# Performance work log

Hardware: AMD Instinct MI355X
Metric: run time of the kernel (lower is better)

The kernel has to match this reference:

```python
import jax, jax.numpy as jnp
import numpy as np

N, K, D, DOUT = 100000, 16, 128, 128

def setup_inputs() -> dict:
    key = jax.random.key(0)
    k1, k2, k3 = jax.random.split(key, 3)
    self_vecs = jax.random.normal(k1, (N, D), dtype=jnp.float32)
    neigh_vecs = jax.random.normal(k2, (N, K, D), dtype=jnp.float32)
    # glorot([input_dim, output_dim])
    limit = np.sqrt(6.0 / (D + DOUT)).astype(np.float32)
    weights = jax.random.uniform(k3, (D, DOUT), dtype=jnp.float32, minval=-limit, maxval=limit)
    return {"self_vecs": self_vecs, "neigh_vecs": neigh_vecs, "weights": weights}

def reference(self_vecs, neigh_vecs, weights):
    # concat self node as an extra "neighbor": [N, K+1, D]
    neigh_self = jnp.concatenate([neigh_vecs, self_vecs[:, None, :]], axis=1)
    # attention scores: query is the self vector, keys are neighbors+self -> [N, K+1]
    score = jnp.einsum('nd,nkd->nk', self_vecs, neigh_self)
    attn = jax.nn.softmax(score, axis=-1)
    # weighted sum of values -> [N, D]
    context = jnp.einsum('nk,nkd->nd', attn, neigh_self)
    out = context @ weights  # [N, DOUT]
    return jax.nn.relu(out)
```

## Files before the change

kernel.cpp:

```cpp
#include <hip/hip_runtime.h>


constexpr int K    = 16;
constexpr int D    = 128;
constexpr int DOUT = 128;
constexpr int WT_PITCH = 136;

typedef short bfrag  __attribute__((ext_vector_type(8)));
typedef float afrag  __attribute__((ext_vector_type(4)));

__device__ __forceinline__ unsigned short f2bf(float f) {
    union { float f; unsigned u; } v; v.f = f;
    const unsigned r = v.u + 0x7FFF + ((v.u >> 16) & 1);
    return (unsigned short)(r >> 16);
}
__device__ __forceinline__ float bf2f(unsigned short b) {
    union { unsigned u; float f; } v; v.u = ((unsigned)b) << 16;
    return v.f;
}

__device__ __forceinline__ float half_allsum(float x) {
    #pragma unroll
    for (int off = 1; off <= 16; off <<= 1)
        x += __shfl_xor(x, off);
    return x;
}

__launch_bounds__(512, 2)
__global__ void gat_fused(const float* __restrict__ self_vecs,
                          const float* __restrict__ neigh_vecs,
                          const float* __restrict__ W,
                          float* __restrict__ out,
                          int n_tiles) {
    __shared__ __align__(16) unsigned short Wt[DOUT][WT_PITCH];
    __shared__ __align__(16) unsigned short Chl[2][2][16][WT_PITCH];

    const int tid = threadIdx.x;

    for (int e = tid; e < D * DOUT; e += blockDim.x) {
        const int k = e >> 7, m = e & 127;
        Wt[m][k] = f2bf(W[e]);
    }
    __syncthreads();

    const int lane = tid & 63;
    const int wid  = tid >> 6;
    const int half = lane >> 5;
    const int q    = lane & 31;
    const int nl   = lane & 15;
    const int kb   = lane >> 4;
    const int r0   = wid * 2;

    float4 v[K], sv;

    int buf = 0;
    int t = blockIdx.x;

    if (t < n_tiles) {
        const int n0 = t * 16 + r0 + half;
        const float4* nb = (const float4*)(neigh_vecs + (size_t)n0 * (K * D)) + q;
        #pragma unroll
        for (int k = 0; k < K; ++k) v[k] = nb[k * 32];
        sv = ((const float4*)(self_vecs + (size_t)n0 * D))[q];
    }

    for (; t < n_tiles; t += gridDim.x, buf ^= 1) {
        const int node0 = t * 16;

        float ss = sv.x * sv.x + sv.y * sv.y + sv.z * sv.z + sv.w * sv.w;
        float sc[K];
        #pragma unroll
        for (int k = 0; k < K; ++k)
            sc[k] = sv.x * v[k].x + sv.y * v[k].y + sv.z * v[k].z + sv.w * v[k].w;
        ss = half_allsum(ss);
        #pragma unroll
        for (int k = 0; k < K; ++k) sc[k] = half_allsum(sc[k]);

        float m = ss;
        #pragma unroll
        for (int k = 0; k < K; ++k) m = fmaxf(m, sc[k]);
        float e   = __expf(ss - m);
        float sum = e;
        float4 cx = make_float4(e * sv.x, e * sv.y, e * sv.z, e * sv.w);
        #pragma unroll
        for (int k = 0; k < K; ++k) {
            const float ek = __expf(sc[k] - m);
            sum += ek;
            cx.x += ek * v[k].x; cx.y += ek * v[k].y;
            cx.z += ek * v[k].z; cx.w += ek * v[k].w;
        }
        const float inv = 1.f / sum;
        const float cf[4] = {cx.x * inv, cx.y * inv, cx.z * inv, cx.w * inv};

        unsigned short hi4[4], lo4[4];
        #pragma unroll
        for (int i = 0; i < 4; ++i) {
            hi4[i] = f2bf(cf[i]);
            lo4[i] = f2bf(cf[i] - bf2f(hi4[i]));
        }
        *(uint2*)&Chl[buf][0][r0 + half][4 * q] = *(const uint2*)hi4;
        *(uint2*)&Chl[buf][1][r0 + half][4 * q] = *(const uint2*)lo4;

        const int tn = t + gridDim.x;
        if (tn < n_tiles) {
            const int n0 = tn * 16 + r0 + half;
            const float4* nb = (const float4*)(neigh_vecs + (size_t)n0 * (K * D)) + q;
            #pragma unroll
            for (int k = 0; k < K; ++k) v[k] = nb[k * 32];
            sv = ((const float4*)(self_vecs + (size_t)n0 * D))[q];
        }

        __syncthreads();

        afrag acc;
        #pragma unroll
        for (int r4 = 0; r4 < 4; ++r4) acc[r4] = 0.f;

        #pragma unroll
        for (int kc = 0; kc < 4; ++kc) {
            const bfrag ch = *(const bfrag*)&Chl[buf][0][nl][kc * 32 + kb * 8];
            const bfrag cl = *(const bfrag*)&Chl[buf][1][nl][kc * 32 + kb * 8];
            const bfrag a  = *(const bfrag*)&Wt[wid * 16 + nl][kc * 32 + kb * 8];
            acc = __builtin_amdgcn_mfma_f32_16x16x32_bf16(a, ch, acc, 0, 0, 0);
            acc = __builtin_amdgcn_mfma_f32_16x16x32_bf16(a, cl, acc, 0, 0, 0);
        }
        float* orow = out + (size_t)(node0 + nl) * DOUT + kb * 4;
        *(float4*)(orow + wid * 16) =
            make_float4(fmaxf(acc[0], 0.f), fmaxf(acc[1], 0.f),
                        fmaxf(acc[2], 0.f), fmaxf(acc[3], 0.f));
    }
}

extern "C" void kernel_launch(void* const* d_in, const int* in_sizes, int n_in,
                              void* d_out, int out_size, void* d_ws, size_t ws_size,
                              hipStream_t stream) {
    const float* self_vecs = (const float*)d_in[0];
    const float* neigh     = (const float*)d_in[1];
    const float* W         = (const float*)d_in[2];
    float* out = (float*)d_out;

    const int n_nodes = in_sizes[0] / D;
    const int n_tiles = n_nodes / 16;

    const int tpb = 512;
    const int blocks = 512;
    gat_fused<<<dim3(blocks), dim3(tpb), 0, stream>>>(
        self_vecs, neigh, W, out, n_tiles);
}
```

Before: 191.7 us.

## Make each wave own a whole 16-node tile, removing block barriers

Each wave now processes a full 16-node tile on its own. It computes the attention context for pairs of nodes with two register sets, so the loads for the next pair overlap the compute of the current one, and then runs all 8 output column tiles of the MFMA GEMM itself. This removes the per-tile __syncthreads and the block-wide double buffer in LDS. The price is higher register pressure from holding two 16-float4 neighbor sets, fewer waves per block (256 threads), and each wave reading all of Wt from LDS.

Measured after the change: 245.9 us. 1.28x slower.

```diff
diff --git a/kernel.cpp b/kernel.cpp
--- a/kernel.cpp
+++ b/kernel.cpp
@@ -26,14 +26,56 @@
     return x;
 }
 
-__launch_bounds__(512, 2)
+#define LOADP(vv, svv, nbase) do {                                              \
+    const int n_ = (nbase) + half;                                              \
+    const float4* nb_ = (const float4*)(neigh_vecs + (size_t)n_ * (K * D)) + q; \
+    _Pragma("unroll")                                                           \
+    for (int k = 0; k < K; ++k) vv[k] = nb_[k * 32];                            \
+    svv = ((const float4*)(self_vecs + (size_t)n_ * D))[q];                     \
+} while (0)
+
+#define CTXPAIR(vv, svv, p) do {                                                \
+    float ss_ = svv.x * svv.x + svv.y * svv.y + svv.z * svv.z + svv.w * svv.w;  \
+    float sc_[K];                                                               \
+    _Pragma("unroll")                                                           \
+    for (int k = 0; k < K; ++k)                                                 \
+        sc_[k] = svv.x * vv[k].x + svv.y * vv[k].y + svv.z * vv[k].z + svv.w * vv[k].w; \
+    ss_ = half_allsum(ss_);                                                     \
+    _Pragma("unroll")                                                           \
+    for (int k = 0; k < K; ++k) sc_[k] = half_allsum(sc_[k]);                   \
+    float m_ = ss_;                                                             \
+    _Pragma("unroll")                                                           \
+    for (int k = 0; k < K; ++k) m_ = fmaxf(m_, sc_[k]);                         \
+    const float e_ = __expf(ss_ - m_);                                          \
+    float sum_ = e_;                                                            \
+    float4 cx_ = make_float4(e_ * svv.x, e_ * svv.y, e_ * svv.z, e_ * svv.w);   \
+    _Pragma("unroll")                                                           \
+    for (int k = 0; k < K; ++k) {                                               \
+        const float ek_ = __expf(sc_[k] - m_);                                  \
+        sum_ += ek_;                                                            \
+        cx_.x += ek_ * vv[k].x; cx_.y += ek_ * vv[k].y;                         \
+        cx_.z += ek_ * vv[k].z; cx_.w += ek_ * vv[k].w;                         \
+    }                                                                           \
+    const float inv_ = 1.f / sum_;                                              \
+    const float cf_[4] = {cx_.x * inv_, cx_.y * inv_, cx_.z * inv_, cx_.w * inv_}; \
+    unsigned short hi4_[4], lo4_[4];                                            \
+    _Pragma("unroll")                                                           \
+    for (int i = 0; i < 4; ++i) {                                               \
+        hi4_[i] = f2bf(cf_[i]);                                                 \
+        lo4_[i] = f2bf(cf_[i] - bf2f(hi4_[i]));                                 \
+    }                                                                           \
+    *(uint2*)&Chl[wid][0][2 * (p) + half][4 * q] = *(const uint2*)hi4_;         \
+    *(uint2*)&Chl[wid][1][2 * (p) + half][4 * q] = *(const uint2*)lo4_;         \
+} while (0)
+
+__launch_bounds__(256, 2)
 __global__ void gat_fused(const float* __restrict__ self_vecs,
                           const float* __restrict__ neigh_vecs,
                           const float* __restrict__ W,
                           float* __restrict__ out,
-                          int n_tiles) {
+                          int n_tiles, int total_waves) {
     __shared__ __align__(16) unsigned short Wt[DOUT][WT_PITCH];
-    __shared__ __align__(16) unsigned short Chl[2][2][16][WT_PITCH];
+    __shared__ __align__(16) unsigned short Chl[4][2][16][WT_PITCH];
 
     const int tid = threadIdx.x;
 
@@ -49,85 +91,53 @@
     const int q    = lane & 31;
     const int nl   = lane & 15;
     const int kb   = lane >> 4;
-    const int r0   = wid * 2;
 
-    float4 v[K], sv;
+    float4 vA[K], vB[K], sA, sB;
 
-    int buf = 0;
-    int t = blockIdx.x;
+    int t = blockIdx.x * 4 + wid;
+    if (t < n_tiles) {
+        LOADP(vA, sA, t * 16 + 0);
+        LOADP(vB, sB, t * 16 + 2);
+    }
+    for (; t < n_tiles; t += total_waves) {
+        const int node0 = t * 16;
+        const int tn = t + total_waves;
 
-    if (t < n_tiles) {
-        const int n0 = t * 16 + r0 + half;
-        const float4* nb = (const float4*)(neigh_vecs + (size_t)n0 * (K * D)) + q;
         #pragma unroll
-        for (int k = 0; k < K; ++k) v[k] = nb[k * 32];
-        sv = ((const float4*)(self_vecs + (size_t)n0 * D))[q];
-    }
-
-    for (; t < n_tiles; t += gridDim.x, buf ^= 1) {
-        const int node0 = t * 16;
-
-        float ss = sv.x * sv.x + sv.y * sv.y + sv.z * sv.z + sv.w * sv.w;
-        float sc[K];
-        #pragma unroll
-        for (int k = 0; k < K; ++k)
-            sc[k] = sv.x * v[k].x + sv.y * v[k].y + sv.z * v[k].z + sv.w * v[k].w;
-        ss = half_allsum(ss);
-        #pragma unroll
-        for (int k = 0; k < K; ++k) sc[k] = half_allsum(sc[k]);
-
-        float m = ss;
-        #pragma unroll
-        for (int k = 0; k < K; ++k) m = fmaxf(m, sc[k]);
-        float e   = __expf(ss - m);
-        float sum = e;
-        float4 cx = make_float4(e * sv.x, e * sv.y, e * sv.z, e * sv.w);
-        #pragma unroll
-        for (int k = 0; k < K; ++k) {
-            const float ek = __expf(sc[k] - m);
-            sum += ek;
-            cx.x += ek * v[k].x; cx.y += ek * v[k].y;
-            cx.z += ek * v[k].z; cx.w += ek * v[k].w;
-        }
-        const float inv = 1.f / sum;
-        const float cf[4] = {cx.x * inv, cx.y * inv, cx.z * inv, cx.w * inv};
-
-        unsigned short hi4[4], lo4[4];
-        #pragma unroll
-        for (int i = 0; i < 4; ++i) {
-            hi4[i] = f2bf(cf[i]);
-            lo4[i] = f2bf(cf[i] - bf2f(hi4[i]));
-        }
-        *(uint2*)&Chl[buf][0][r0 + half][4 * q] = *(const uint2*)hi4;
-        *(uint2*)&Chl[buf][1][r0 + half][4 * q] = *(const uint2*)lo4;
-
-        const int tn = t + gridDim.x;
-        if (tn < n_tiles) {
-            const int n0 = tn * 16 + r0 + half;
-            const float4* nb = (const float4*)(neigh_vecs + (size_t)n0 * (K * D)) + q;
-            #pragma unroll
-            for (int k = 0; k < K; ++k) v[k] = nb[k * 32];
-            sv = ((const float4*)(self_vecs + (size_t)n0 * D))[q];
+        for (int p = 0; p < 8; ++p) {
+            if ((p & 1) == 0) {
+                CTXPAIR(vA, sA, p);
+                if (p + 2 < 8)            LOADP(vA, sA, node0 + 2 * (p + 2));
+                else if (tn < n_tiles)    LOADP(vA, sA, tn * 16 + 0);
+            } else {
+                CTXPAIR(vB, sB, p);
+                if (p + 2 < 8)            LOADP(vB, sB, node0 + 2 * (p + 2));
+                else if (tn < n_tiles)    LOADP(vB, sB, tn * 16 + 2);
+            }
         }
 
-        __syncthreads();
-
-        afrag acc;
-        #pragma unroll
-        for (int r4 = 0; r4 < 4; ++r4) acc[r4] = 0.f;
-
+        bfrag ch[4], cl[4];
         #pragma unroll
         for (int kc = 0; kc < 4; ++kc) {
-            const bfrag ch = *(const bfrag*)&Chl[buf][0][nl][kc * 32 + kb * 8];
-            const bfrag cl = *(const bfrag*)&Chl[buf][1][nl][kc * 32 + kb * 8];
-            const bfrag a  = *(const bfrag*)&Wt[wid * 16 + nl][kc * 32 + kb * 8];
-            acc = __builtin_amdgcn_mfma_f32_16x16x32_bf16(a, ch, acc, 0, 0, 0);
-            acc = __builtin_amdgcn_mfma_f32_16x16x32_bf16(a, cl, acc, 0, 0, 0);
+            ch[kc] = *(const bfrag*)&Chl[wid][0][nl][kc * 32 + kb * 8];
+            cl[kc] = *(const bfrag*)&Chl[wid][1][nl][kc * 32 + kb * 8];
         }
         float* orow = out + (size_t)(node0 + nl) * DOUT + kb * 4;
-        *(float4*)(orow + wid * 16) =
-            make_float4(fmaxf(acc[0], 0.f), fmaxf(acc[1], 0.f),
-                        fmaxf(acc[2], 0.f), fmaxf(acc[3], 0.f));
+        #pragma unroll
+        for (int nt = 0; nt < 8; ++nt) {
+            afrag acc;
+            #pragma unroll
+            for (int r4 = 0; r4 < 4; ++r4) acc[r4] = 0.f;
+            #pragma unroll
+            for (int kc = 0; kc < 4; ++kc) {
+                const bfrag a = *(const bfrag*)&Wt[nt * 16 + nl][kc * 32 + kb * 8];
+                acc = __builtin_amdgcn_mfma_f32_16x16x32_bf16(a, ch[kc], acc, 0, 0, 0);
+                acc = __builtin_amdgcn_mfma_f32_16x16x32_bf16(a, cl[kc], acc, 0, 0, 0);
+            }
+            *(float4*)(orow + nt * 16) =
+                make_float4(fmaxf(acc[0], 0.f), fmaxf(acc[1], 0.f),
+                            fmaxf(acc[2], 0.f), fmaxf(acc[3], 0.f));
+        }
     }
 }
 
@@ -142,8 +152,9 @@
     const int n_nodes = in_sizes[0] / D;
     const int n_tiles = n_nodes / 16;
 
-    const int tpb = 512;
+    const int tpb = 256;
     const int blocks = 512;
+    const int total_waves = blocks * (tpb / 64);
     gat_fused<<<dim3(blocks), dim3(tpb), 0, stream>>>(
-        self_vecs, neigh, W, out, n_tiles);
+        self_vecs, neigh, W, out, n_tiles, total_waves);
 }
```
